# Optimization experiments

Hardware: AMD Instinct MI355X
Metric: run time of the kernel (lower is better)

The kernel has to match this reference:

```python
import jax, jax.numpy as jnp
import numpy as np

D_MODEL = 512
D_STATE = 128
D_CONV = 4
EXPAND = 2
NL = 10
HEADDIM = 64
D_INNER = EXPAND * D_MODEL            # 1024
NHEADS = D_INNER // HEADDIM           # 16
CONV_DIM = D_INNER + 2 * D_STATE      # 1280
D_PROJ = 2 * D_INNER + 2 * D_STATE + NHEADS  # 2320
BATCH = 8
IN_S, TOK_S = 3647, 64                # -> 57 tokens
IN_G, TOK_G = 18, 2                   # -> 9 tokens
NCLS = 55
CA_HEADS = 8
EPS = 1e-5


def setup_inputs() -> dict:
    key = jax.random.key(0)
    ks = iter(jax.random.split(key, 80))
    nrm = lambda shape, s=0.02: jax.random.normal(next(ks), shape, jnp.float32) * s
    inp = {
        "x_spectra": jax.random.normal(next(ks), (BATCH, IN_S), jnp.float32),
        "x_gaia": jax.random.normal(next(ks), (BATCH, IN_G), jnp.float32),
        "tok_w_s": nrm((TOK_S, D_MODEL), 0.05), "tok_b_s": jnp.zeros((D_MODEL,)),
        "tok_w_g": nrm((TOK_G, D_MODEL), 0.05), "tok_b_g": jnp.zeros((D_MODEL,)),
    }
    for p in ("ms", "mg"):  # spectra / gaia Mamba2 stacks, params stacked over layers
        inp[p + "_Win"] = nrm((NL, D_MODEL, D_PROJ))
        inp[p + "_conv_w"] = nrm((NL, CONV_DIM, D_CONV), 0.1)
        inp[p + "_conv_b"] = jnp.zeros((NL, CONV_DIM))
        inp[p + "_dt_bias"] = nrm((NL, NHEADS), 0.5)
        inp[p + "_A_log"] = jnp.log(jnp.tile(jnp.arange(1, NHEADS + 1, dtype=jnp.float32), (NL, 1)))
        inp[p + "_D"] = jnp.ones((NL, NHEADS))
        inp[p + "_norm_w"] = jnp.ones((NL, D_INNER))
        inp[p + "_Wout"] = nrm((NL, D_INNER, D_MODEL))
    for p in ("ca_s", "ca_g"):  # cross-attention blocks
        inp[p + "_ln_w"] = jnp.ones((D_MODEL,)); inp[p + "_ln_b"] = jnp.zeros((D_MODEL,))
        inp[p + "_in_w"] = nrm((3 * D_MODEL, D_MODEL)); inp[p + "_in_b"] = jnp.zeros((3 * D_MODEL,))
        inp[p + "_out_w"] = nrm((D_MODEL, D_MODEL)); inp[p + "_out_b"] = jnp.zeros((D_MODEL,))
    inp["cls_ln_w"] = jnp.ones((2 * D_MODEL,)); inp["cls_ln_b"] = jnp.zeros((2 * D_MODEL,))
    inp["cls_w"] = nrm((NCLS, 2 * D_MODEL)); inp["cls_b"] = jnp.zeros((NCLS,))
    return inp


def _ln(x, w, b):
    m = x.mean(-1, keepdims=True)
    v = jnp.var(x, -1, keepdims=True)
    return (x - m) * jax.lax.rsqrt(v + EPS) * w + b


def _tokenize(x, in_dim, tok_dim, w, b):
    bsz = x.shape[0]
    ntok = -(-in_dim // tok_dim)
    x = jnp.pad(x, ((0, 0), (0, ntok * tok_dim - in_dim)))
    return x.reshape(bsz, ntok, tok_dim) @ w + b  # [B, ntok, d_model]


def _mamba2_layer(x, Win, conv_w, conv_b, dt_bias, A_log, Dp, norm_w, Wout):
    bsz, L, _ = x.shape
    zxbcdt = x @ Win  # [B,L,D_PROJ]
    z, xBC, dt = jnp.split(zxbcdt, [D_INNER, D_INNER + CONV_DIM], axis=-1)
    # causal depthwise conv over time (kernel D_CONV), then SiLU
    xp = jnp.pad(xBC, ((0, 0), (D_CONV - 1, 0), (0, 0)))
    xBC = sum(conv_w[:, k] * xp[:, k:k + L, :] for k in range(D_CONV)) + conv_b
    xBC = jax.nn.silu(xBC)
    xh, Bm, Cm = jnp.split(xBC, [D_INNER, D_INNER + D_STATE], axis=-1)
    dt = jax.nn.softplus(dt + dt_bias)                 # [B,L,H]
    A = -jnp.exp(A_log)                                # [H]
    xh = xh.reshape(bsz, L, NHEADS, HEADDIM)
    dA = jnp.exp(dt * A)                               # [B,L,H] in (0,1)
    dBx = jnp.einsum('blh,bln,blhp->blhpn', dt, Bm, xh)
    # h_t = dA_t * h_{t-1} + dBx_t  via parallel associative scan over time
    def comb(e1, e2):
        a1, b1 = e1
        a2, b2 = e2
        return a1 * a2, a2[..., None, None] * b1 + b2
    _, h = jax.lax.associative_scan(comb, (dA, dBx), axis=1)  # h: [B,L,H,P,N]
    y = jnp.einsum('blhpn,bln->blhp', h, Cm) + Dp[None, None, :, None] * xh
    y = y.reshape(bsz, L, D_INNER)
    # gated RMSNorm (norm_before_gate=False): rmsnorm(y * silu(z)) * w
    y = y * jax.nn.silu(z)
    y = y * jax.lax.rsqrt(jnp.mean(y * y, -1, keepdims=True) + EPS) * norm_w
    return y @ Wout


def _mamba_stack(x, Win, cw, cb, dtb, Alog, Dp, nw, Wout):
    for i in range(NL):
        x = _mamba2_layer(x, Win[i], cw[i], cb[i], dtb[i], Alog[i], Dp[i], nw[i], Wout[i])
    return x


def _mha(q, kv, in_w, in_b, out_w, out_b):
    E = D_MODEL
    hd = E // CA_HEADS
    wq, wk, wv = in_w[:E], in_w[E:2 * E], in_w[2 * E:]
    bq, bk, bv = in_b[:E], in_b[E:2 * E], in_b[2 * E:]
    qh = (q @ wq.T + bq).reshape(*q.shape[:2], CA_HEADS, hd)
    kh = (kv @ wk.T + bk).reshape(*kv.shape[:2], CA_HEADS, hd)
    vh = (kv @ wv.T + bv).reshape(*kv.shape[:2], CA_HEADS, hd)
    scores = jnp.einsum('bqhd,bkhd->bhqk', qh, kh) / np.sqrt(hd).astype(np.float32)
    attn = jax.nn.softmax(scores, axis=-1)
    out = jnp.einsum('bhqk,bkhd->bqhd', attn, vh).reshape(*q.shape[:2], E)
    return out @ out_w.T + out_b


def reference(x_spectra, x_gaia, tok_w_s, tok_b_s, tok_w_g, tok_b_g,
              ms_Win, ms_conv_w, ms_conv_b, ms_dt_bias, ms_A_log, ms_D, ms_norm_w, ms_Wout,
              mg_Win, mg_conv_w, mg_conv_b, mg_dt_bias, mg_A_log, mg_D, mg_norm_w, mg_Wout,
              ca_s_ln_w, ca_s_ln_b, ca_s_in_w, ca_s_in_b, ca_s_out_w, ca_s_out_b,
              ca_g_ln_w, ca_g_ln_b, ca_g_in_w, ca_g_in_b, ca_g_out_w, ca_g_out_b,
              cls_ln_w, cls_ln_b, cls_w, cls_b):
    xs = _tokenize(x_spectra, IN_S, TOK_S, tok_w_s, tok_b_s)   # [B,57,512]
    xg = _tokenize(x_gaia, IN_G, TOK_G, tok_w_g, tok_b_g)      # [B,9,512]
    xs = _mamba_stack(xs, ms_Win, ms_conv_w, ms_conv_b, ms_dt_bias, ms_A_log, ms_D, ms_norm_w, ms_Wout)
    xg = _mamba_stack(xg, mg_Win, mg_conv_w, mg_conv_b, mg_dt_bias, mg_A_log, mg_D, mg_norm_w, mg_Wout)
    # cross attention (note: gaia attends to the UPDATED spectra, as in the torch code)
    xs = xs + _mha(_ln(xs, ca_s_ln_w, ca_s_ln_b), xg, ca_s_in_w, ca_s_in_b, ca_s_out_w, ca_s_out_b)
    xg = xg + _mha(_ln(xg, ca_g_ln_w, ca_g_ln_b), xs, ca_g_in_w, ca_g_in_b, ca_g_out_w, ca_g_out_b)
    fused = jnp.concatenate([xs.mean(1), xg.mean(1)], axis=-1)  # [B,1024]
    return _ln(fused, cls_ln_w, cls_ln_b) @ cls_w.T + cls_b      # [B,55]
```

## Files before the change

kernel.cpp:

```cpp
#include <hip/hip_runtime.h>
#include <cmath>

constexpr int BB    = 8;
constexpr int LS    = 57;
constexpr int LG    = 9;
constexpr int RS    = BB*LS;
constexpr int RG    = BB*LG;
constexpr int DM    = 512;
constexpr int DPROJ = 2320;
constexpr int DIN   = 1024;
constexpr int NH    = 16;
constexpr int HD    = 64;
constexpr int NLAY  = 10;

constexpr int SP_IN  = 2;
constexpr int SP_OUT = 8;
constexpr int SP_ATT = 4;

__device__ __forceinline__ float siluf(float x){ return x / (1.f + expf(-x)); }

typedef short  short8  __attribute__((ext_vector_type(8)));
typedef short  short4_ __attribute__((ext_vector_type(4)));
typedef float  f32x4   __attribute__((ext_vector_type(4)));

__device__ __forceinline__ unsigned short f2bh(float f){
    unsigned int u = __float_as_uint(f);
    u = u + 0x7FFFu + ((u >> 16) & 1u);
    return (unsigned short)(u >> 16);
}
__device__ __forceinline__ float bh2f(unsigned short h){
    return __uint_as_float(((unsigned int)h) << 16);
}

__global__ __launch_bounds__(512) void tokenize2(
    const float* __restrict__ xS, const float* __restrict__ wS, const float* __restrict__ bS,
    float* __restrict__ oS, unsigned short* __restrict__ oSh, unsigned short* __restrict__ oSl,
    const float* __restrict__ xG, const float* __restrict__ wG, const float* __restrict__ bG,
    float* __restrict__ oG, unsigned short* __restrict__ oGh, unsigned short* __restrict__ oGl)
{
    const int st = blockIdx.z;
    const int tkt = blockIdx.x, b = blockIdx.y, d = threadIdx.x;
    const int ntok = st ? LG : LS;
    if (tkt >= ntok) return;
    const float* x = st ? xG : xS;
    const float* w = st ? wG : wS;
    const float* bias = st ? bG : bS;
    float* out = st ? oG : oS;
    unsigned short* oh = st ? oGh : oSh;
    unsigned short* ol = st ? oGl : oSl;
    const int in_dim = st ? 18 : 3647, tok_dim = st ? 2 : 64;

    __shared__ float xv[64];
    if (d < tok_dim) {
        int idx = tkt*tok_dim + d;
        xv[d] = (idx < in_dim) ? x[(size_t)b*in_dim + idx] : 0.f;
    }
    __syncthreads();
    float acc = bias[d];
    for (int k=0;k<tok_dim;k++) acc += xv[k]*w[(size_t)k*DM + d];
    const size_t o = (size_t)(b*ntok + tkt)*DM + d;
    out[o] = acc;
    const unsigned short h = f2bh(acc);
    oh[o] = h;
    ol[o] = f2bh(acc - bh2f(h));
}

struct CvtE { const float* src; unsigned short* h; unsigned short* l; int nblk; };

__global__ __launch_bounds__(256) void convert_weights(
    const float* __restrict__ winS, const float* __restrict__ winG,
    const float* __restrict__ woutS, const float* __restrict__ woutG,
    unsigned short* __restrict__ winh, unsigned short* __restrict__ winl,
    unsigned short* __restrict__ wouth, unsigned short* __restrict__ woutl,
    CvtE e0, CvtE e1, CvtE e2, CvtE e3)
{
    __shared__ float tile[64][65];
    const int tid = threadIdx.x;
    const int bid = blockIdx.x;

    const float* src; unsigned short *dh, *dl; int K, N, nt, kt;
    if (bid < 5920){
        const int plane = bid / 296, rem = bid % 296;
        const int s = plane & 1, layer = plane >> 1;
        src = (s ? winG : winS) + (size_t)layer*DM*DPROJ;
        dh = winh + (size_t)plane*DPROJ*DM;
        dl = winl + (size_t)plane*DPROJ*DM;
        K = DM; N = DPROJ;
        nt = (rem % 37)*64; kt = (rem / 37)*64;
    } else if (bid < 8480){
        const int i = bid - 5920;
        const int plane = i / 128, rem = i % 128;
        const int s = plane & 1, layer = plane >> 1;
        src = (s ? woutG : woutS) + (size_t)layer*DIN*DM;
        dh = wouth + (size_t)plane*DM*DIN;
        dl = woutl + (size_t)plane*DM*DIN;
        K = DIN; N = DM;
        nt = (rem % 8)*64; kt = (rem / 8)*64;
    } else {
        int e = bid - 8480;
        CvtE j;
        if (e < e0.nblk){ j = e0; }
        else if (e < e0.nblk + e1.nblk){ j = e1; e -= e0.nblk; }
        else if (e < e0.nblk + e1.nblk + e2.nblk){ j = e2; e -= e0.nblk + e1.nblk; }
        else { j = e3; e -= e0.nblk + e1.nblk + e2.nblk; }
        const int i4 = (e*256 + tid)*4;
        const float4 v = *(const float4*)(j.src + i4);
        const float f[4] = {v.x,v.y,v.z,v.w};
        short4_ h4, l4;
        #pragma unroll
        for (int q=0;q<4;q++){
            const unsigned short h = f2bh(f[q]);
            h4[q] = (short)h;
            l4[q] = (short)f2bh(f[q] - bh2f(h));
        }
        *(short4_*)(j.h + i4) = h4;
        *(short4_*)(j.l + i4) = l4;
        return;
    }

    #pragma unroll
    for (int i=0;i<4;i++){
        const int kk = (tid>>4) + i*16;
        const int c4 = (tid&15)*4;
        const int n = nt + c4;
        float4 v = {0.f,0.f,0.f,0.f};
        if (n + 3 < N) v = *(const float4*)(src + (size_t)(kt+kk)*N + n);
        else {
            if (n   < N) v.x = src[(size_t)(kt+kk)*N + n];
            if (n+1 < N) v.y = src[(size_t)(kt+kk)*N + n+1];
            if (n+2 < N) v.z = src[(size_t)(kt+kk)*N + n+2];
            if (n+3 < N) v.w = src[(size_t)(kt+kk)*N + n+3];
        }
        tile[kk][c4]=v.x; tile[kk][c4+1]=v.y; tile[kk][c4+2]=v.z; tile[kk][c4+3]=v.w;
    }
    __syncthreads();
    #pragma unroll
    for (int i=0;i<2;i++){
        const int c = tid + i*256;
        const int n = c >> 3, k8 = (c & 7)*8;
        if (nt + n < N){
            short8 vh_, vl_;
            #pragma unroll
            for (int q=0;q<8;q++){
                const float f = tile[k8+q][n];
                const unsigned short h = f2bh(f);
                vh_[q] = (short)h;
                vl_[q] = (short)f2bh(f - bh2f(h));
            }
            *(short8*)(dh + (size_t)(nt+n)*K + kt + k8) = vh_;
            *(short8*)(dl + (size_t)(nt+n)*K + kt + k8) = vl_;
        }
    }
}

struct GemmJob {
    const unsigned short* Ah; const unsigned short* Al;
    const unsigned short* Wh; const unsigned short* Wl;
    float* part; int M;
};

template<int NSPLIT>
__global__ __launch_bounds__(256) void gemm_mfma(GemmJob j0, GemmJob j1, GemmJob j2, int N, int K)
{
    const int z = blockIdx.z;
    const int job = z / NSPLIT, split = z % NSPLIT;
    GemmJob jb = (job==0) ? j0 : (job==1 ? j1 : j2);
    const int bm = blockIdx.y*64, bn = blockIdx.x*64;
    const int M = jb.M;
    if (bm >= M) return;

    constexpr int SR = 40;
    __shared__ unsigned short AhS[2][64*SR], AlS[2][64*SR];
    __shared__ unsigned short BhS[2][64*SR], BlS[2][64*SR];

    const int tid = threadIdx.x;
    const int r0 = tid >> 2, k0off = (tid & 3)*8;
    const bool aok = (bm + r0 < M);
    const bool wok = (bn + r0 < N);
    const unsigned short* Aph = jb.Ah + (size_t)(bm+r0)*K;
    const unsigned short* Apl = jb.Al + (size_t)(bm+r0)*K;
    const unsigned short* Wph = jb.Wh + (size_t)(bn+r0)*K;
    const unsigned short* Wpl = jb.Wl + (size_t)(bn+r0)*K;

    const short8 z8 = {0,0,0,0,0,0,0,0};
    short8 ra_h = z8, ra_l = z8, rw_h = z8, rw_l = z8;

    auto loadT = [&](int k0){
        if (aok){
            ra_h = *(const short8*)(Aph + k0 + k0off);
            ra_l = *(const short8*)(Apl + k0 + k0off);
        } else { ra_h = z8; ra_l = z8; }
        if (wok){
            rw_h = *(const short8*)(Wph + k0 + k0off);
            rw_l = *(const short8*)(Wpl + k0 + k0off);
        } else { rw_h = z8; rw_l = z8; }
    };
    auto storeT = [&](int buf){
        *(short8*)&AhS[buf][r0*SR + k0off] = ra_h;
        *(short8*)&AlS[buf][r0*SR + k0off] = ra_l;
        *(short8*)&BhS[buf][r0*SR + k0off] = rw_h;
        *(short8*)&BlS[buf][r0*SR + k0off] = rw_l;
    };

    const int Kper = K / NSPLIT;
    const int koff = split * Kper;
    const int nk = Kper / 32;

    const int l = tid & 63, w = tid >> 6;
    const int fr = l & 15, kg = (l >> 4)*8;

    f32x4 acc0 = {0.f,0.f,0.f,0.f};
    f32x4 acc1 = {0.f,0.f,0.f,0.f};
    f32x4 acc2 = {0.f,0.f,0.f,0.f};
    f32x4 acc3 = {0.f,0.f,0.f,0.f};

    loadT(koff);
    storeT(0);
    __syncthreads();
    for (int t=0; t<nk; ++t){
        const int cur = t & 1;
        if (t+1 < nk) loadT(koff + (t+1)*32);

        const short8 ah = *(const short8*)&AhS[cur][(w*16+fr)*SR + kg];
        const short8 al = *(const short8*)&AlS[cur][(w*16+fr)*SR + kg];
        {
            const short8 bh = *(const short8*)&BhS[cur][(fr)*SR + kg];
            const short8 bl = *(const short8*)&BlS[cur][(fr)*SR + kg];
            acc0 = __builtin_amdgcn_mfma_f32_16x16x32_bf16(ah, bh, acc0, 0,0,0);
            acc0 = __builtin_amdgcn_mfma_f32_16x16x32_bf16(ah, bl, acc0, 0,0,0);
            acc0 = __builtin_amdgcn_mfma_f32_16x16x32_bf16(al, bh, acc0, 0,0,0);
        }
        {
            const short8 bh = *(const short8*)&BhS[cur][(16+fr)*SR + kg];
            const short8 bl = *(const short8*)&BlS[cur][(16+fr)*SR + kg];
            acc1 = __builtin_amdgcn_mfma_f32_16x16x32_bf16(ah, bh, acc1, 0,0,0);
            acc1 = __builtin_amdgcn_mfma_f32_16x16x32_bf16(ah, bl, acc1, 0,0,0);
            acc1 = __builtin_amdgcn_mfma_f32_16x16x32_bf16(al, bh, acc1, 0,0,0);
        }
        {
            const short8 bh = *(const short8*)&BhS[cur][(32+fr)*SR + kg];
            const short8 bl = *(const short8*)&BlS[cur][(32+fr)*SR + kg];
            acc2 = __builtin_amdgcn_mfma_f32_16x16x32_bf16(ah, bh, acc2, 0,0,0);
            acc2 = __builtin_amdgcn_mfma_f32_16x16x32_bf16(ah, bl, acc2, 0,0,0);
            acc2 = __builtin_amdgcn_mfma_f32_16x16x32_bf16(al, bh, acc2, 0,0,0);
        }
        {
            const short8 bh = *(const short8*)&BhS[cur][(48+fr)*SR + kg];
            const short8 bl = *(const short8*)&BlS[cur][(48+fr)*SR + kg];
            acc3 = __builtin_amdgcn_mfma_f32_16x16x32_bf16(ah, bh, acc3, 0,0,0);
            acc3 = __builtin_amdgcn_mfma_f32_16x16x32_bf16(ah, bl, acc3, 0,0,0);
            acc3 = __builtin_amdgcn_mfma_f32_16x16x32_bf16(al, bh, acc3, 0,0,0);
        }
        if (t+1 < nk) storeT(cur^1);
        __syncthreads();
    }

    float* __restrict__ P = jb.part + (size_t)split*M*N;
    const int rbase = bm + w*16 + (l>>4)*4;
    #pragma unroll
    for (int nt=0; nt<4; ++nt){
        const f32x4 a = (nt==0)?acc0 : (nt==1)?acc1 : (nt==2)?acc2 : acc3;
        const int n = bn + nt*16 + fr;
        if (n < N){
            #pragma unroll
            for (int j=0;j<4;j++){
                const int m = rbase + j;
                if (m < M) P[(size_t)m*N + n] = a[j];
            }
        }
    }
}

struct RJob { const float* part; const float* bias; const float* res; float* C;
              unsigned short* ph; unsigned short* pl; int M; };

template<int NS>
__global__ __launch_bounds__(256) void reduce_k(RJob j0, RJob j1, int N)
{
    RJob j = blockIdx.y ? j1 : j0;
    const size_t total = (size_t)j.M*N;
    const size_t i4 = ((size_t)blockIdx.x*256 + threadIdx.x)*4;
    if (i4 >= total) return;
    float4 s = *(const float4*)(j.part + i4);
    #pragma unroll
    for (int t=1;t<NS;t++){
        const float4 v = *(const float4*)(j.part + (size_t)t*total + i4);
        s.x+=v.x; s.y+=v.y; s.z+=v.z; s.w+=v.w;
    }
    const int n = (int)(i4 % (size_t)N);
    if (j.bias){ s.x+=j.bias[n]; s.y+=j.bias[n+1]; s.z+=j.bias[n+2]; s.w+=j.bias[n+3]; }
    if (j.res){ const float4 r = *(const float4*)(j.res + i4); s.x+=r.x; s.y+=r.y; s.z+=r.z; s.w+=r.w; }
    if (j.C) *(float4*)(j.C + i4) = s;
    if (j.ph){
        const float f[4] = {s.x, s.y, s.z, s.w};
        short4_ h4, l4;
        #pragma unroll
        for (int q=0;q<4;q++){
            const unsigned short h = f2bh(f[q]);
            h4[q] = (short)h;
            l4[q] = (short)f2bh(f[q] - bh2f(h));
        }
        *(short4_*)(j.ph + i4) = h4;
        *(short4_*)(j.pl + i4) = l4;
    }
}

struct PrepJob {
    const float* part;
    float* zsilu; float* xh; float* Bc; float* Cc; float* dtw;
    const float* cw; const float* cb; const float* dtb;
    int R, L;
};

__device__ __forceinline__ float4 psum2(const float* p, size_t pstr){
    float4 a = *(const float4*)p;
    const float4 b = *(const float4*)(p + pstr);
    a.x += b.x; a.y += b.y; a.z += b.z; a.w += b.w;
    return a;
}

__global__ __launch_bounds__(256) void mamba_prep(PrepJob js, PrepJob jg)
{
    PrepJob j = blockIdx.y ? jg : js;
    const int R = j.R, L = j.L;
    constexpr int QPR = 580;
    const int q = blockIdx.x*256 + threadIdx.x;
    if (q >= R*QPR) return;
    const int r = q / QPR, qi = q % QPR;
    const int l = r % L;
    const size_t pstr = (size_t)R*DPROJ;
    const float* base = j.part + (size_t)r*DPROJ;

    if (qi < 256) {
        const int c = qi*4;
        float4 s = psum2(base + c, pstr);
        s.x = siluf(s.x); s.y = siluf(s.y); s.z = siluf(s.z); s.w = siluf(s.w);
        *(float4*)(j.zsilu + (size_t)r*1024 + c) = s;
    } else if (qi < 576) {
        const int cc = (qi-256)*4;
        float tk[4][4];
        #pragma unroll
        for (int k=0;k<4;k++){
            const int lr = l - 3 + k;
            if (lr >= 0){
                float4 v = psum2(j.part + (size_t)(r-3+k)*DPROJ + 1024 + cc, pstr);
                tk[k][0]=v.x; tk[k][1]=v.y; tk[k][2]=v.z; tk[k][3]=v.w;
            } else {
                tk[k][0]=0.f; tk[k][1]=0.f; tk[k][2]=0.f; tk[k][3]=0.f;
            }
        }
        const float4 cb4 = *(const float4*)(j.cb + cc);
        const float cba[4] = {cb4.x, cb4.y, cb4.z, cb4.w};
        float out[4];
        #pragma unroll
        for (int jj=0;jj<4;jj++){
            const float4 wv = *(const float4*)(j.cw + (size_t)(cc+jj)*4);
            float v = cba[jj] + wv.x*tk[0][jj] + wv.y*tk[1][jj]
                              + wv.z*tk[2][jj] + wv.w*tk[3][jj];
            out[jj] = siluf(v);
        }
        float4 o4; o4.x=out[0]; o4.y=out[1]; o4.z=out[2]; o4.w=out[3];
        if (cc < 1024)       *(float4*)(j.xh + (size_t)r*1024 + cc)        = o4;
        else if (cc < 1152)  *(float4*)(j.Bc + (size_t)r*128 + (cc-1024))  = o4;
        else                 *(float4*)(j.Cc + (size_t)r*128 + (cc-1152))  = o4;
    } else {
        const int hd = (qi-576)*4;
        float4 s = psum2(base + 2304 + hd, pstr);
        const float4 b4 = *(const float4*)(j.dtb + hd);
        float raw[4] = {s.x+b4.x, s.y+b4.y, s.z+b4.z, s.w+b4.w};
        float4 o4;
        float* op = &o4.x;
        #pragma unroll
        for (int jj=0;jj<4;jj++)
            op[jj] = (raw[jj] > 20.f) ? raw[jj] : log1pf(expf(raw[jj]));
        *(float4*)(j.dtw + (size_t)r*16 + hd) = o4;
    }
}

__global__ __launch_bounds__(256) void mamba_cbt(
    const float* __restrict__ Bc_s, const float* __restrict__ Cc_s, float* __restrict__ cbt_s,
    const float* __restrict__ Bc_g, const float* __restrict__ Cc_g, float* __restrict__ cbt_g)
{
    const int b = blockIdx.x, st = blockIdx.y;
    const float* Bc = st ? Bc_g : Bc_s;
    const float* Cc = st ? Cc_g : Cc_s;
    float* cbt = st ? cbt_g : cbt_s;
    const int L = st ? LG : LS;
    constexpr int SB = 132;
    __shared__ float Bm[64*SB], Cm[64*SB];
    const int t = threadIdx.x;
    for (int idx = t; idx < L*32; idx += 256){
        const int l = idx >> 5, c4 = (idx & 31)*4;
        *(float4*)&Bm[l*SB + c4] = *(const float4*)(Bc + (size_t)(b*L+l)*128 + c4);
        *(float4*)&Cm[l*SB + c4] = *(const float4*)(Cc + (size_t)(b*L+l)*128 + c4);
    }
    __syncthreads();
    const int ti = t >> 4, tj = t & 15;
    float acc[4][4] = {};
    for (int k0=0;k0<128;k0+=4){
        float4 cr[4], br[4];
        #pragma unroll
        for (int a=0;a<4;a++) cr[a] = *(const float4*)&Cm[(ti+16*a)*SB + k0];
        #pragma unroll
        for (int qq=0;qq<4;qq++) br[qq] = *(const float4*)&Bm[(tj+16*qq)*SB + k0];
        #pragma unroll
        for (int a=0;a<4;a++)
            #pragma unroll
            for (int qq=0;qq<4;qq++)
                acc[a][qq] += cr[a].x*br[qq].x + cr[a].y*br[qq].y
                            + cr[a].z*br[qq].z + cr[a].w*br[qq].w;
    }
    #pragma unroll
    for (int a=0;a<4;a++){
        const int i = ti + 16*a;
        if (i < L){
            #pragma unroll
            for (int qq=0;qq<4;qq++){
                const int jj = tj + 16*qq;
                if (jj < L) cbt[(size_t)b*3840 + i*60 + jj] = acc[a][qq];
// ... 40 lines not shown
        *(float4*)&Xm[l*SX + c4] = *(const float4*)(xh + (size_t)(b*L+l)*1024 + h*64 + c4);
    }
    __syncthreads();

    for (int idx = t; idx < L*15; idx += 256){
        const int i = idx/15, j4 = (idx%15)*4;
        const float4 v = *(const float4*)(cbt + (size_t)b*3840 + i*60 + j4);
        const float va[4] = {v.x, v.y, v.z, v.w};
        float g[4];
        const float si = sps[i];
        #pragma unroll
        for (int jj=0;jj<4;jj++){
            const int jc = j4 + jj;
            float gg = 0.f;
            if (jc <= i && jc < L)
                gg = expf(Ah*(si - sps[jc])) * dts[jc] * va[jj];
            g[jj] = gg;
        }
        float4 g4; g4.x=g[0]; g4.y=g[1]; g4.z=g[2]; g4.w=g[3];
        *(float4*)&Gm[i*SG + j4] = g4;
    }
    __syncthreads();

    const int ti = t >> 4, tj = t & 15;
    int la[4];
    #pragma unroll
    for (int a=0;a<4;a++) la[a] = ti + 16*a;
    float accY[4][4] = {};
    for (int m=0; m<L; ++m){
        float xr[4], gr[4];
        #pragma unroll
        for (int qq=0;qq<4;qq++) xr[qq] = Xm[m*SX + tj + 16*qq];
        #pragma unroll
        for (int a=0;a<4;a++) gr[a] = (la[a] < L) ? Gm[la[a]*SG + m] : 0.f;
        #pragma unroll
        for (int a=0;a<4;a++)
            #pragma unroll
            for (int qq=0;qq<4;qq++) accY[a][qq] = fmaf(gr[a], xr[qq], accY[a][qq]);
    }
    #pragma unroll
    for (int a=0;a<4;a++){
        if (la[a] < L){
            float* yrow = y + (size_t)(b*L + la[a])*DIN + h*HD;
            #pragma unroll
            for (int qq=0;qq<4;qq++){
                const int col = tj + 16*qq;
                yrow[col] = accY[a][qq] + Dh * Xm[la[a]*SX + col];
            }
        }
    }
}

__global__ __launch_bounds__(256) void gated_rmsnorm(
    const float* __restrict__ y_s, const float* __restrict__ zs_s, const float* __restrict__ nw_s,
    unsigned short* __restrict__ oh_s, unsigned short* __restrict__ ol_s,
    const float* __restrict__ y_g, const float* __restrict__ zs_g, const float* __restrict__ nw_g,
    unsigned short* __restrict__ oh_g, unsigned short* __restrict__ ol_g)
{
    int r = blockIdx.x, t = threadIdx.x;
    int st = (r >= RS);
    int row = st ? r - RS : r;
    const float* y  = (st ? y_g  : y_s) + (size_t)row*DIN;
    const float* zs = (st ? zs_g : zs_s) + (size_t)row*DIN;
    const float* nw = st ? nw_g : nw_s;
    unsigned short* oh = (st ? oh_g : oh_s) + (size_t)row*DIN;
    unsigned short* ol = (st ? ol_g : ol_s) + (size_t)row*DIN;

    float g[4]; float s2 = 0.f;
    #pragma unroll
    for (int i=0;i<4;i++){
        int idx = t + i*256;
        float gv = y[idx] * zs[idx];
        g[i] = gv; s2 += gv*gv;
    }
    #pragma unroll
    for (int o2=32;o2;o2>>=1) s2 += __shfl_xor(s2, o2, 64);
    __shared__ float red[4];
    if ((t & 63) == 0) red[t>>6] = s2;
    __syncthreads();
    float S2 = red[0]+red[1]+red[2]+red[3];
    float scale = rsqrtf(S2*(1.f/DIN) + 1e-5f);
    #pragma unroll
    for (int i=0;i<4;i++){
        int idx = t + i*256;
        const float val = g[i]*scale*nw[idx];
        const unsigned short h = f2bh(val);
        oh[idx] = h;
        ol[idx] = f2bh(val - bh2f(h));
    }
}

__global__ __launch_bounds__(256) void ln_rows(
    const float* __restrict__ x, const float* __restrict__ w, const float* __restrict__ b,
    unsigned short* __restrict__ outh, unsigned short* __restrict__ outl, int D)
{
    int r = blockIdx.x, t = threadIdx.x;
    const float* xr = x + (size_t)r*D;
    float s = 0.f, s2 = 0.f;
    for (int i=t;i<D;i+=256){ float v = xr[i]; s += v; s2 += v*v; }
    #pragma unroll
    for (int o=32;o;o>>=1){ s += __shfl_xor(s,o,64); s2 += __shfl_xor(s2,o,64); }
    __shared__ float red[8];
    if ((t & 63) == 0){ red[t>>6] = s; red[4+(t>>6)] = s2; }
    __syncthreads();
    float S  = red[0]+red[1]+red[2]+red[3];
    float S2 = red[4]+red[5]+red[6]+red[7];
    float mean = S/D;
    float var  = S2/D - mean*mean;
    float inv  = rsqrtf(var + 1e-5f);
    for (int i=t;i<D;i+=256){
        const float val = (xr[i]-mean)*inv*w[i] + b[i];
        const unsigned short h = f2bh(val);
        outh[(size_t)r*D + i] = h;
        outl[(size_t)r*D + i] = f2bh(val - bh2f(h));
    }
}

template<int LQ, int LKV, int NS>
__global__ __launch_bounds__(256) void mha_attn2(
    const float* __restrict__ pq, const float* __restrict__ pk, const float* __restrict__ pv,
    const float* __restrict__ qb, const float* __restrict__ kb, const float* __restrict__ vb,
    int Mq, int Mkv,
    unsigned short* __restrict__ outh, unsigned short* __restrict__ outl)
{
    const int hh = blockIdx.x, b = blockIdx.y, t = threadIdx.x;
// ... 182 lines not shown
    (void)in_sizes; (void)n_in; (void)out_size; (void)ws_size;
    const float* x_spectra = (const float*)d_in[0];
    const float* x_gaia    = (const float*)d_in[1];
    const float* tok_w_s   = (const float*)d_in[2];
    const float* tok_b_s   = (const float*)d_in[3];
    const float* tok_w_g   = (const float*)d_in[4];
    const float* tok_b_g   = (const float*)d_in[5];
    const float* ms_Win    = (const float*)d_in[6];
    const float* ms_conv_w = (const float*)d_in[7];
    const float* ms_conv_b = (const float*)d_in[8];
    const float* ms_dtb    = (const float*)d_in[9];
    const float* ms_Alog   = (const float*)d_in[10];
    const float* ms_D      = (const float*)d_in[11];
    const float* ms_nw     = (const float*)d_in[12];
    const float* ms_Wout   = (const float*)d_in[13];
    const float* mg_Win    = (const float*)d_in[14];
    const float* mg_conv_w = (const float*)d_in[15];
    const float* mg_conv_b = (const float*)d_in[16];
    const float* mg_dtb    = (const float*)d_in[17];
    const float* mg_Alog   = (const float*)d_in[18];
    const float* mg_D      = (const float*)d_in[19];
    const float* mg_nw     = (const float*)d_in[20];
    const float* mg_Wout   = (const float*)d_in[21];
    const float* cas_ln_w  = (const float*)d_in[22];
    const float* cas_ln_b  = (const float*)d_in[23];
    const float* cas_in_w  = (const float*)d_in[24];
    const float* cas_in_b  = (const float*)d_in[25];
    const float* cas_out_w = (const float*)d_in[26];
    const float* cas_out_b = (const float*)d_in[27];
    const float* cag_ln_w  = (const float*)d_in[28];
    const float* cag_ln_b  = (const float*)d_in[29];
    const float* cag_in_w  = (const float*)d_in[30];
    const float* cag_in_b  = (const float*)d_in[31];
    const float* cag_out_w = (const float*)d_in[32];
    const float* cag_out_b = (const float*)d_in[33];
    const float* cls_ln_w  = (const float*)d_in[34];
    const float* cls_ln_b  = (const float*)d_in[35];
    const float* cls_w     = (const float*)d_in[36];
    const float* cls_b     = (const float*)d_in[37];

    float* p = (float*)d_ws;
    auto alloc = [&](size_t n){ float* r = p; p += n; return r; };
    float* xs       = alloc((size_t)RS*DM);
    float* xg       = alloc((size_t)RG*DM);
    float* y_s      = alloc((size_t)RS*DIN);
    float* y_g      = alloc((size_t)RG*DIN);
    float* part_inS  = alloc((size_t)SP_IN*RS*DPROJ);
    float* part_inG  = alloc((size_t)SP_IN*RG*DPROJ);
    float* part_outS = alloc((size_t)SP_OUT*RS*DM);
    float* part_outG = alloc((size_t)SP_OUT*RG*DM);
    float* part_q    = alloc((size_t)SP_ATT*RS*DM);
    float* part_k    = alloc((size_t)SP_ATT*RS*DM);
    float* part_v    = alloc((size_t)SP_ATT*RS*DM);
    float* zsilu_s = alloc((size_t)RS*1024);
    float* zsilu_g = alloc((size_t)RG*1024);
    float* xh_s    = alloc((size_t)RS*1024);
    float* xh_g    = alloc((size_t)RG*1024);
    float* Bc_s    = alloc((size_t)RS*128);
    float* Bc_g    = alloc((size_t)RG*128);
    float* Cc_s    = alloc((size_t)RS*128);
    float* Cc_g    = alloc((size_t)RG*128);
    float* dtw_s   = alloc((size_t)RS*16);
    float* dtw_g   = alloc((size_t)RG*16);
    float* cbt_s   = alloc((size_t)BB*3840);
    float* cbt_g   = alloc((size_t)BB*3840);

    unsigned short* up = (unsigned short*)p;
    auto ualloc = [&](size_t n){ unsigned short* r = up; up += n; return r; };
    unsigned short* xsh   = ualloc((size_t)RS*DM);
    unsigned short* xsl   = ualloc((size_t)RS*DM);
    unsigned short* xgh   = ualloc((size_t)RG*DM);
    unsigned short* xgl   = ualloc((size_t)RG*DM);
    unsigned short* ynh_s = ualloc((size_t)RS*DIN);
    unsigned short* ynl_s = ualloc((size_t)RS*DIN);
    unsigned short* ynh_g = ualloc((size_t)RG*DIN);
    unsigned short* ynl_g = ualloc((size_t)RG*DIN);
    unsigned short* lnh   = ualloc((size_t)RS*DM);
    unsigned short* lnl   = ualloc((size_t)RS*DM);
    unsigned short* aoh   = ualloc((size_t)RS*DM);
    unsigned short* aol   = ualloc((size_t)RS*DM);
    unsigned short* caih  = ualloc((size_t)1536*512);
    unsigned short* cail  = ualloc((size_t)1536*512);
    unsigned short* caoh  = ualloc((size_t)512*512);
    unsigned short* caol  = ualloc((size_t)512*512);
    unsigned short* cgih  = ualloc((size_t)1536*512);
    unsigned short* cgil  = ualloc((size_t)1536*512);
    unsigned short* cgoh  = ualloc((size_t)512*512);
    unsigned short* cgol  = ualloc((size_t)512*512);
    unsigned short* winh  = ualloc((size_t)20*DPROJ*DM);
    unsigned short* winl  = ualloc((size_t)20*DPROJ*DM);
    unsigned short* wouth = ualloc((size_t)20*DM*DIN);
    unsigned short* woutl = ualloc((size_t)20*DM*DIN);

    CvtE e0{cas_in_w,  caih, cail, 768};
    CvtE e1{cas_out_w, caoh, caol, 256};
    CvtE e2{cag_in_w,  cgih, cgil, 768};
    CvtE e3{cag_out_w, cgoh, cgol, 256};
    convert_weights<<<dim3(10528), 256, 0, stream>>>(
        ms_Win, mg_Win, ms_Wout, mg_Wout, winh, winl, wouth, woutl, e0, e1, e2, e3);

    tokenize2<<<dim3(LS, BB, 2), 512, 0, stream>>>(
        x_spectra, tok_w_s, tok_b_s, xs, xsh, xsl,
        x_gaia,    tok_w_g, tok_b_g, xg, xgh, xgl);

    const int rblkS = (RS*DM + 1023)/1024;
    const int prepBlk = (RS*580 + 255)/256;

    for (int i=0;i<NLAY;i++){
        const float* cw_s   = ms_conv_w + (size_t)i*1280*4;
        const float* cw_g   = mg_conv_w + (size_t)i*1280*4;
        const float* cbv_s  = ms_conv_b + (size_t)i*1280;
        const float* cbv_g  = mg_conv_b + (size_t)i*1280;
        const float* dtb_s  = ms_dtb  + (size_t)i*NH;
        const float* dtb_g  = mg_dtb  + (size_t)i*NH;
        const float* al_s   = ms_Alog + (size_t)i*NH;
        const float* al_g   = mg_Alog + (size_t)i*NH;
        const float* Dw_s   = ms_D    + (size_t)i*NH;
        const float* Dw_g   = mg_D    + (size_t)i*NH;
        const float* nw_s   = ms_nw   + (size_t)i*DIN;
        const float* nw_g   = mg_nw   + (size_t)i*DIN;

        const unsigned short* wih_s = winh + (size_t)(2*i+0)*DPROJ*DM;
        const unsigned short* wil_s = winl + (size_t)(2*i+0)*DPROJ*DM;
        const unsigned short* wih_g = winh + (size_t)(2*i+1)*DPROJ*DM;
        const unsigned short* wil_g = winl + (size_t)(2*i+1)*DPROJ*DM;
        const unsigned short* woh_s = wouth + (size_t)(2*i+0)*DM*DIN;
        const unsigned short* wol_s = woutl + (size_t)(2*i+0)*DM*DIN;
        const unsigned short* woh_g = wouth + (size_t)(2*i+1)*DM*DIN;
        const unsigned short* wol_g = woutl + (size_t)(2*i+1)*DM*DIN;

        GemmJob inS{xsh, xsl, wih_s, wil_s, part_inS, RS};
        GemmJob inG{xgh, xgl, wih_g, wil_g, part_inG, RG};
        gemm_mfma<SP_IN><<<dim3(37, 8, 2*SP_IN), 256, 0, stream>>>(inS, inG, inG, DPROJ, DM);

        PrepJob pjS{part_inS, zsilu_s, xh_s, Bc_s, Cc_s, dtw_s, cw_s, cbv_s, dtb_s, RS, LS};
        PrepJob pjG{part_inG, zsilu_g, xh_g, Bc_g, Cc_g, dtw_g, cw_g, cbv_g, dtb_g, RG, LG};
        mamba_prep<<<dim3(prepBlk, 2), 256, 0, stream>>>(pjS, pjG);

        mamba_cbt<<<dim3(BB, 2), 256, 0, stream>>>(Bc_s, Cc_s, cbt_s, Bc_g, Cc_g, cbt_g);

        mamba_y<<<dim3(NH, BB, 2), 256, 0, stream>>>(
            cbt_s, xh_s, dtw_s, al_s, Dw_s, y_s,
            cbt_g, xh_g, dtw_g, al_g, Dw_g, y_g);

        gated_rmsnorm<<<dim3(RS+RG), 256, 0, stream>>>(
            y_s, zsilu_s, nw_s, ynh_s, ynl_s,  y_g, zsilu_g, nw_g, ynh_g, ynl_g);

        GemmJob outS{ynh_s, ynl_s, woh_s, wol_s, part_outS, RS};
        GemmJob outG{ynh_g, ynl_g, woh_g, wol_g, part_outG, RG};
        gemm_mfma<SP_OUT><<<dim3(8, 8, 2*SP_OUT), 256, 0, stream>>>(outS, outG, outG, DM, DIN);

        RJob roS{part_outS, nullptr, nullptr, xs, xsh, xsl, RS};
        RJob roG{part_outG, nullptr, nullptr, xg, xgh, xgl, RG};
        reduce_k<SP_OUT><<<dim3(rblkS, 2), 256, 0, stream>>>(roS, roG, DM);
    }

    {
        ln_rows<<<dim3(RS), 256, 0, stream>>>(xs, cas_ln_w, cas_ln_b, lnh, lnl, DM);
        GemmJob jq{lnh, lnl, caih,            cail,            part_q, RS};
        GemmJob jk{xgh, xgl, caih +  512*512, cail +  512*512, part_k, RG};
        GemmJob jv{xgh, xgl, caih + 1024*512, cail + 1024*512, part_v, RG};
        gemm_mfma<SP_ATT><<<dim3(8, 8, 3*SP_ATT), 256, 0, stream>>>(jq, jk, jv, DM, DM);
        mha_attn2<LS,LG,SP_ATT><<<dim3(8,BB), 256, 0, stream>>>(
            part_q, part_k, part_v, cas_in_b, cas_in_b+512, cas_in_b+1024, RS, RG, aoh, aol);
        GemmJob jo{aoh, aol, caoh, caol, part_outS, RS};
        gemm_mfma<SP_ATT><<<dim3(8, 8, SP_ATT), 256, 0, stream>>>(jo, jo, jo, DM, DM);
        RJob ro{part_outS, cas_out_b, xs, xs, xsh, xsl, RS};
        reduce_k<SP_ATT><<<dim3(rblkS, 1), 256, 0, stream>>>(ro, ro, DM);
    }

    {
        ln_rows<<<dim3(RG), 256, 0, stream>>>(xg, cag_ln_w, cag_ln_b, lnh, lnl, DM);
        GemmJob jq{lnh, lnl, cgih,            cgil,            part_q, RG};
        GemmJob jk{xsh, xsl, cgih +  512*512, cgil +  512*512, part_k, RS};
        GemmJob jv{xsh, xsl, cgih + 1024*512, cgil + 1024*512, part_v, RS};
        gemm_mfma<SP_ATT><<<dim3(8, 8, 3*SP_ATT), 256, 0, stream>>>(jq, jk, jv, DM, DM);
        mha_attn2<LG,LS,SP_ATT><<<dim3(8,BB), 256, 0, stream>>>(
            part_q, part_k, part_v, cag_in_b, cag_in_b+512, cag_in_b+1024, RG, RS, aoh, aol);
        GemmJob jo{aoh, aol, cgoh, cgol, part_outS, RG};
        gemm_mfma<SP_ATT><<<dim3(8, 2, SP_ATT), 256, 0, stream>>>(jo, jo, jo, DM, DM);
        RJob ro{part_outS, cag_out_b, xg, xg, nullptr, nullptr, RG};
        reduce_k<SP_ATT><<<dim3((RG*DM+1023)/1024, 1), 256, 0, stream>>>(ro, ro, DM);
    }

    head_fused<<<dim3(BB), 512, 0, stream>>>(xs, xg, cls_ln_w, cls_ln_b, cls_w, cls_b, (float*)d_out);
}
```

Before: 749.7 us.

## Pre-tile bf16 weight planes for contiguous GEMM loads and fuse z-silu into rmsnorm

```diff
diff --git a/kernel.cpp b/kernel.cpp
--- a/kernel.cpp
+++ b/kernel.cpp
@@ -17,6 +17,13 @@
 constexpr int SP_OUT = 8;
 constexpr int SP_ATT = 4;
 
+constexpr int NT_IN  = 37;
+constexpr int NT_OUT = 8;
+constexpr int NT_ATT = 8;
+constexpr size_t WIN_PLANE  = (size_t)16*NT_IN*2048;
+constexpr size_t WOUT_PLANE = (size_t)32*NT_OUT*2048;
+constexpr size_t ATT_PLANE  = (size_t)16*NT_ATT*2048;
+
 __device__ __forceinline__ float siluf(float x){ return x / (1.f + expf(-x)); }
 
 typedef short  short8  __attribute__((ext_vector_type(8)));
@@ -65,91 +72,97 @@
     ol[o] = f2bh(acc - bh2f(h));
 }
 
-struct CvtE { const float* src; unsigned short* h; unsigned short* l; int nblk; };
-
 __global__ __launch_bounds__(256) void convert_weights(
     const float* __restrict__ winS, const float* __restrict__ winG,
     const float* __restrict__ woutS, const float* __restrict__ woutG,
+    const float* __restrict__ cai, const float* __restrict__ cao,
+    const float* __restrict__ cgi, const float* __restrict__ cgo,
     unsigned short* __restrict__ winh, unsigned short* __restrict__ winl,
     unsigned short* __restrict__ wouth, unsigned short* __restrict__ woutl,
-    CvtE e0, CvtE e1, CvtE e2, CvtE e3)
-{
-    __shared__ float tile[64][65];
+    unsigned short* __restrict__ atth, unsigned short* __restrict__ attl)
+{
     const int tid = threadIdx.x;
     const int bid = blockIdx.x;
 
-    const float* src; unsigned short *dh, *dl; int K, N, nt, kt;
+    if (bid >= 8480){
+        int e = bid - 8480;
+        const int job = e >> 7, rem = e & 127;
+        const int kt2 = rem >> 3, nt2 = rem & 7;
+        const float* src =
+            (job==3) ? cao : (job==7) ? cgo :
+            (job< 3) ? cai + (size_t)job*512*512 : cgi + (size_t)(job-4)*512*512;
+        const size_t tile = (size_t)job*ATT_PLANE + ((size_t)kt2*NT_ATT + nt2)*2048;
+        const int n = tid >> 2, k8 = (tid & 3)*8;
+        const float* sp = src + (size_t)(nt2*64 + n)*512 + kt2*32 + k8;
+        const float4 v0 = *(const float4*)sp;
+        const float4 v1 = *(const float4*)(sp+4);
+        const float f[8] = {v0.x,v0.y,v0.z,v0.w,v1.x,v1.y,v1.z,v1.w};
+        short8 h8, l8;
+        #pragma unroll
+        for (int q=0;q<8;q++){
+            const unsigned short h = f2bh(f[q]);
+            h8[q] = (short)h;
+            l8[q] = (short)f2bh(f[q] - bh2f(h));
+        }
+        *(short8*)(atth + tile + tid*8) = h8;
+        *(short8*)(attl + tile + tid*8) = l8;
+        return;
+    }
+
+    const float* src; unsigned short *dh, *dl; int K, N, NT, nt, ktp;
     if (bid < 5920){
         const int plane = bid / 296, rem = bid % 296;
         const int s = plane & 1, layer = plane >> 1;
         src = (s ? winG : winS) + (size_t)layer*DM*DPROJ;
-        dh = winh + (size_t)plane*DPROJ*DM;
-        dl = winl + (size_t)plane*DPROJ*DM;
-        K = DM; N = DPROJ;
-        nt = (rem % 37)*64; kt = (rem / 37)*64;
-    } else if (bid < 8480){
+        dh = winh + (size_t)plane*WIN_PLANE;
+        dl = winl + (size_t)plane*WIN_PLANE;
+        K = DM; N = DPROJ; NT = NT_IN;
+        nt = rem % 37; ktp = rem / 37;
+    } else {
         const int i = bid - 5920;
         const int plane = i / 128, rem = i % 128;
         const int s = plane & 1, layer = plane >> 1;
         src = (s ? woutG : woutS) + (size_t)layer*DIN*DM;
-        dh = wouth + (size_t)plane*DM*DIN;
-        dl = woutl + (size_t)plane*DM*DIN;
-        K = DIN; N = DM;
-        nt = (rem % 8)*64; kt = (rem / 8)*64;
-    } else {
-        int e = bid - 8480;
-        CvtE j;
-        if (e < e0.nblk){ j = e0; }
-        else if (e < e0.nblk + e1.nblk){ j = e1; e -= e0.nblk; }
-        else if (e < e0.nblk + e1.nblk + e2.nblk){ j = e2; e -= e0.nblk + e1.nblk; }
-        else { j = e3; e -= e0.nblk + e1.nblk + e2.nblk; }
-        const int i4 = (e*256 + tid)*4;
-        const float4 v = *(const float4*)(j.src + i4);
-        const float f[4] = {v.x,v.y,v.z,v.w};
-        short4_ h4, l4;
-        #pragma unroll
-        for (int q=0;q<4;q++){
-            const unsigned short h = f2bh(f[q]);
-            h4[q] = (short)h;
-            l4[q] = (short)f2bh(f[q] - bh2f(h));
-        }
-        *(short4_*)(j.h + i4) = h4;
-        *(short4_*)(j.l + i4) = l4;
-        return;
-    }
-
+        dh = wouth + (size_t)plane*WOUT_PLANE;
+        dl = woutl + (size_t)plane*WOUT_PLANE;
+        K = DIN; N = DM; NT = NT_OUT;
+        nt = rem % 8; ktp = rem / 8;
+    }
+
+    __shared__ float tile[64][66];
     #pragma unroll
     for (int i=0;i<4;i++){
         const int kk = (tid>>4) + i*16;
         const int c4 = (tid&15)*4;
-        const int n = nt + c4;
+        const int n = nt*64 + c4;
         float4 v = {0.f,0.f,0.f,0.f};
-        if (n + 3 < N) v = *(const float4*)(src + (size_t)(kt+kk)*N + n);
+        const float* sp = src + (size_t)(ktp*64+kk)*N + n;
+        if (n + 3 < N) v = *(const float4*)sp;
         else {
-            if (n   < N) v.x = src[(size_t)(kt+kk)*N + n];
-            if (n+1 < N) v.y = src[(size_t)(kt+kk)*N + n+1];
-            if (n+2 < N) v.z = src[(size_t)(kt+kk)*N + n+2];
-            if (n+3 < N) v.w = src[(size_t)(kt+kk)*N + n+3];
+            if (n   < N) v.x = sp[0];
+            if (n+1 < N) v.y = sp[1];
+            if (n+2 < N) v.z = sp[2];
+            if (n+3 < N) v.w = sp[3];
         }
         tile[kk][c4]=v.x; tile[kk][c4+1]=v.y; tile[kk][c4+2]=v.z; tile[kk][c4+3]=v.w;
     }
     __syncthreads();
+
+    const int n_l = tid >> 2, k8 = (tid & 3)*8;
     #pragma unroll
     for (int i=0;i<2;i++){
-        const int c = tid + i*256;
-        const int n = c >> 3, k8 = (c & 7)*8;
-        if (nt + n < N){
-            short8 vh_, vl_;
-            #pragma unroll
-            for (int q=0;q<8;q++){
-                const float f = tile[k8+q][n];
-                const unsigned short h = f2bh(f);
-                vh_[q] = (short)h;
-                vl_[q] = (short)f2bh(f - bh2f(h));
-            }
-            *(short8*)(dh + (size_t)(nt+n)*K + kt + k8) = vh_;
-            *(short8*)(dl + (size_t)(nt+n)*K + kt + k8) = vl_;
-        }
+        const int kt2 = ktp*2 + i;
+        short8 h8, l8;
+        #pragma unroll
+        for (int q=0;q<8;q++){
+            const float f = tile[i*32 + k8 + q][n_l];
+            const unsigned short h = f2bh(f);
+            h8[q] = (short)h;
+            l8[q] = (short)f2bh(f - bh2f(h));
+        }
+        const size_t off = ((size_t)kt2*NT + nt)*2048 + tid*8;
+        *(short8*)(dh + off) = h8;
+        *(short8*)(dl + off) = l8;
     }
 }
 
@@ -160,12 +173,13 @@
 };
 
 template<int NSPLIT>
-__global__ __launch_bounds__(256) void gemm_mfma(GemmJob j0, GemmJob j1, GemmJob j2, int N, int K)
+__global__ __launch_bounds__(256) void gemm_mfma(GemmJob j0, GemmJob j1, GemmJob j2,
+                                                 int N, int K, int NT)
 {
     const int z = blockIdx.z;
     const int job = z / NSPLIT, split = z % NSPLIT;
     GemmJob jb = (job==0) ? j0 : (job==1 ? j1 : j2);
-    const int bm = blockIdx.y*64, bn = blockIdx.x*64;
+    const int bm = blockIdx.y*64, bn64 = blockIdx.x;
     const int M = jb.M;
     if (bm >= M) return;
 
@@ -176,24 +190,26 @@
     const int tid = threadIdx.x;
     const int r0 = tid >> 2, k0off = (tid & 3)*8;
     const bool aok = (bm + r0 < M);
-    const bool wok = (bn + r0 < N);
     const unsigned short* Aph = jb.Ah + (size_t)(bm+r0)*K;
     const unsigned short* Apl = jb.Al + (size_t)(bm+r0)*K;
-    const unsigned short* Wph = jb.Wh + (size_t)(bn+r0)*K;
-    const unsigned short* Wpl = jb.Wl + (size_t)(bn+r0)*K;
+
+    const int Kper = K / NSPLIT;
+    const int koff = split * Kper;
+    const int nk = Kper / 32;
+
+    const size_t wbase = ((size_t)(koff >> 5)*NT + bn64)*2048 + (size_t)tid*8;
+    const size_t wstep = (size_t)NT*2048;
 
     const short8 z8 = {0,0,0,0,0,0,0,0};
     short8 ra_h = z8, ra_l = z8, rw_h = z8, rw_l = z8;
 
-    auto loadT = [&](int k0){
+    auto loadT = [&](int k0, int tstep){
         if (aok){
             ra_h = *(const short8*)(Aph + k0 + k0off);
             ra_l = *(const short8*)(Apl + k0 + k0off);
         } else { ra_h = z8; ra_l = z8; }
-        if (wok){
-            rw_h = *(const short8*)(Wph + k0 + k0off);
-            rw_l = *(const short8*)(Wpl + k0 + k0off);
-        } else { rw_h = z8; rw_l = z8; }
+        rw_h = *(const short8*)(jb.Wh + wbase + (size_t)tstep*wstep);
+        rw_l = *(const short8*)(jb.Wl + wbase + (size_t)tstep*wstep);
     };
     auto storeT = [&](int buf){
         *(short8*)&AhS[buf][r0*SR + k0off] = ra_h;
@@ -202,10 +218,6 @@
         *(short8*)&BlS[buf][r0*SR + k0off] = rw_l;
     };
 
-    const int Kper = K / NSPLIT;
-    const int koff = split * Kper;
-    const int nk = Kper / 32;
-
     const int l = tid & 63, w = tid >> 6;
     const int fr = l & 15, kg = (l >> 4)*8;
 
@@ -214,12 +226,12 @@
     f32x4 acc2 = {0.f,0.f,0.f,0.f};
     f32x4 acc3 = {0.f,0.f,0.f,0.f};
 
-    loadT(koff);
+    loadT(koff, 0);
     storeT(0);
     __syncthreads();
     for (int t=0; t<nk; ++t){
         const int cur = t & 1;
-        if (t+1 < nk) loadT(koff + (t+1)*32);
+        if (t+1 < nk) loadT(koff + (t+1)*32, t+1);
 
         const short8 ah = *(const short8*)&AhS[cur][(w*16+fr)*SR + kg];
         const short8 al = *(const short8*)&AlS[cur][(w*16+fr)*SR + kg];
@@ -257,6 +269,7 @@
 
     float* __restrict__ P = jb.part + (size_t)split*M*N;
     const int rbase = bm + w*16 + (l>>4)*4;
+    const int bn = bn64*64;
     #pragma unroll
     for (int nt=0; nt<4; ++nt){
         const f32x4 a = (nt==0)?acc0 : (nt==1)?acc1 : (nt==2)?acc2 : acc3;
@@ -307,7 +320,7 @@
 
 struct PrepJob {
     const float* part;
-    float* zsilu; float* xh; float* Bc; float* Cc; float* dtw;
+    float* xh; float* Bc; float* Cc; float* dtw;
     const float* cw; const float* cb; const float* dtb;
     int R, L;
 };
@@ -323,7 +336,7 @@
 {
     PrepJob j = blockIdx.y ? jg : js;
     const int R = j.R, L = j.L;
-    constexpr int QPR = 580;
+    constexpr int QPR = 324;
     const int q = blockIdx.x*256 + threadIdx.x;
     if (q >= R*QPR) return;
     const int r = q / QPR, qi = q % QPR;
@@ -331,13 +344,8 @@
     const size_t pstr = (size_t)R*DPROJ;
     const float* base = j.part + (size_t)r*DPROJ;
 
-    if (qi < 256) {
-        const int c = qi*4;
-        float4 s = psum2(base + c, pstr);
-        s.x = siluf(s.x); s.y = siluf(s.y); s.z = siluf(s.z); s.w = siluf(s.w);
-        *(float4*)(j.zsilu + (size_t)r*1024 + c) = s;
-    } else if (qi < 576) {
-        const int cc = (qi-256)*4;
+    if (qi < 320) {
+        const int cc = qi*4;
         float tk[4][4];
         #pragma unroll
         for (int k=0;k<4;k++){
@@ -364,7 +372,7 @@
         else if (cc < 1152)  *(float4*)(j.Bc + (size_t)r*128 + (cc-1024))  = o4;
         else                 *(float4*)(j.Cc + (size_t)r*128 + (cc-1152))  = o4;
     } else {
-        const int hd = (qi-576)*4;
+        const int hd = (qi-320)*4;
         float4 s = psum2(base + 2304 + hd, pstr);
         const float4 b4 = *(const float4*)(j.dtb + hd);
         float raw[4] = {s.x+b4.x, s.y+b4.y, s.z+b4.z, s.w+b4.w};
@@ -511,16 +519,17 @@
 }
 
 __global__ __launch_bounds__(256) void gated_rmsnorm(
-    const float* __restrict__ y_s, const float* __restrict__ zs_s, const float* __restrict__ nw_s,
+    const float* __restrict__ y_s, const float* __restrict__ part_s, const float* __restrict__ nw_s,
     unsigned short* __restrict__ oh_s, unsigned short* __restrict__ ol_s,
-    const float* __restrict__ y_g, const float* __restrict__ zs_g, const float* __restrict__ nw_g,
+    const float* __restrict__ y_g, const float* __restrict__ part_g, const float* __restrict__ nw_g,
     unsigned short* __restrict__ oh_g, unsigned short* __restrict__ ol_g)
 {
     int r = blockIdx.x, t = threadIdx.x;
     int st = (r >= RS);
     int row = st ? r - RS : r;
     const float* y  = (st ? y_g  : y_s) + (size_t)row*DIN;
-    const float* zs = (st ? zs_g : zs_s) + (size_t)row*DIN;
+    const float* zp = (st ? part_g : part_s) + (size_t)row*DPROJ;
+    const size_t pstr = (size_t)(st ? RG : RS)*DPROJ;
     const float* nw = st ? nw_g : nw_s;
     unsigned short* oh = (st ? oh_g : oh_s) + (size_t)row*DIN;
     unsigned short* ol = (st ? ol_g : ol_s) + (size_t)row*DIN;
@@ -529,7 +538,8 @@
     #pragma unroll
     for (int i=0;i<4;i++){
         int idx = t + i*256;
-        float gv = y[idx] * zs[idx];
+        const float zv = zp[idx] + zp[pstr + idx];
+        float gv = y[idx] * siluf(zv);
         g[i] = gv; s2 += gv*gv;
     }
     #pragma unroll
@@ -818,8 +828,6 @@
     float* part_q    = alloc((size_t)SP_ATT*RS*DM);
     float* part_k    = alloc((size_t)SP_ATT*RS*DM);
     float* part_v    = alloc((size_t)SP_ATT*RS*DM);
-    float* zsilu_s = alloc((size_t)RS*1024);
-    float* zsilu_g = alloc((size_t)RG*1024);
     float* xh_s    = alloc((size_t)RS*1024);
     float* xh_g    = alloc((size_t)RG*1024);
     float* Bc_s    = alloc((size_t)RS*128);
@@ -845,32 +853,33 @@
     unsigned short* lnl   = ualloc((size_t)RS*DM);
     unsigned short* aoh   = ualloc((size_t)RS*DM);
     unsigned short* aol   = ualloc((size_t)RS*DM);
-    unsigned short* caih  = ualloc((size_t)1536*512);
-    unsigned short* cail  = ualloc((size_t)1536*512);
-    unsigned short* caoh  = ualloc((size_t)512*512);
-    unsigned short* caol  = ualloc((size_t)512*512);
-    unsigned short* cgih  = ualloc((size_t)1536*512);
-    unsigned short* cgil  = ualloc((size_t)1536*512);
-    unsigned short* cgoh  = ualloc((size_t)512*512);
-    unsigned short* cgol  = ualloc((size_t)512*512);
-    unsigned short* winh  = ualloc((size_t)20*DPROJ*DM);
-    unsigned short* winl  = ualloc((size_t)20*DPROJ*DM);
-    unsigned short* wouth = ualloc((size_t)20*DM*DIN);
-    unsigned short* woutl = ualloc((size_t)20*DM*DIN);
-
-    CvtE e0{cas_in_w,  caih, cail, 768};
-    CvtE e1{cas_out_w, caoh, caol, 256};
-    CvtE e2{cag_in_w,  cgih, cgil, 768};
-    CvtE e3{cag_out_w, cgoh, cgol, 256};
-    convert_weights<<<dim3(10528), 256, 0, stream>>>(
-        ms_Win, mg_Win, ms_Wout, mg_Wout, winh, winl, wouth, woutl, e0, e1, e2, e3);
+    unsigned short* atth  = ualloc((size_t)8*ATT_PLANE);
+    unsigned short* attl  = ualloc((size_t)8*ATT_PLANE);
+    unsigned short* winh  = ualloc((size_t)20*WIN_PLANE);
+    unsigned short* winl  = ualloc((size_t)20*WIN_PLANE);
+    unsigned short* wouth = ualloc((size_t)20*WOUT_PLANE);
+    unsigned short* woutl = ualloc((size_t)20*WOUT_PLANE);
+
+    unsigned short* casq_h = atth + 0*ATT_PLANE; unsigned short* casq_l = attl + 0*ATT_PLANE;
+    unsigned short* cask_h = atth + 1*ATT_PLANE; unsigned short* cask_l = attl + 1*ATT_PLANE;
+    unsigned short* casv_h = atth + 2*ATT_PLANE; unsigned short* casv_l = attl + 2*ATT_PLANE;
+    unsigned short* caso_h = atth + 3*ATT_PLANE; unsigned short* caso_l = attl + 3*ATT_PLANE;
+    unsigned short* cagq_h = atth + 4*ATT_PLANE; unsigned short* cagq_l = attl + 4*ATT_PLANE;
+    unsigned short* cagk_h = atth + 5*ATT_PLANE; unsigned short* cagk_l = attl + 5*ATT_PLANE;
+    unsigned short* cagv_h = atth + 6*ATT_PLANE; unsigned short* cagv_l = attl + 6*ATT_PLANE;
+    unsigned short* cago_h = atth + 7*ATT_PLANE; unsigned short* cago_l = attl + 7*ATT_PLANE;
+
+    convert_weights<<<dim3(9504), 256, 0, stream>>>(
+        ms_Win, mg_Win, ms_Wout, mg_Wout,
+        cas_in_w, cas_out_w, cag_in_w, cag_out_w,
+        winh, winl, wouth, woutl, atth, attl);
 
     tokenize2<<<dim3(LS, BB, 2), 512, 0, stream>>>(
         x_spectra, tok_w_s, tok_b_s, xs, xsh, xsl,
         x_gaia,    tok_w_g, tok_b_g, xg, xgh, xgl);
 
     const int rblkS = (RS*DM + 1023)/1024;
-    const int prepBlk = (RS*580 + 255)/256;
+    const int prepBlk = (RS*324 + 255)/256;
 
     for (int i=0;i<NLAY;i++){
         const float* cw_s   = ms_conv_w + (size_t)i*1280*4;
@@ -886,21 +895,22 @@
         const float* nw_s   = ms_nw   + (size_t)i*DIN;
         const float* nw_g   = mg_nw   + (size_t)i*DIN;
 
-        const unsigned short* wih_s = winh + (size_t)(2*i+0)*DPROJ*DM;
-        const unsigned short* wil_s = winl + (size_t)(2*i+0)*DPROJ*DM;
-        const unsigned short* wih_g = winh + (size_t)(2*i+1)*DPROJ*DM;
-        const unsigned short* wil_g = winl + (size_t)(2*i+1)*DPROJ*DM;
-        const unsigned short* woh_s = wouth + (size_t)(2*i+0)*DM*DIN;
-        const unsigned short* wol_s = woutl + (size_t)(2*i+0)*DM*DIN;
-        const unsigned short* woh_g = wouth + (size_t)(2*i+1)*DM*DIN;
-        const unsigned short* wol_g = woutl + (size_t)(2*i+1)*DM*DIN;
+        const unsigned short* wih_s = winh + (size_t)(2*i+0)*WIN_PLANE;
+        const unsigned short* wil_s = winl + (size_t)(2*i+0)*WIN_PLANE;
+        const unsigned short* wih_g = winh + (size_t)(2*i+1)*WIN_PLANE;
+        const unsigned short* wil_g = winl + (size_t)(2*i+1)*WIN_PLANE;
+        const unsigned short* woh_s = wouth + (size_t)(2*i+0)*WOUT_PLANE;
+        const unsigned short* wol_s = woutl + (size_t)(2*i+0)*WOUT_PLANE;
+        const unsigned short* woh_g = wouth + (size_t)(2*i+1)*WOUT_PLANE;
+        const unsigned short* wol_g = woutl + (size_t)(2*i+1)*WOUT_PLANE;
 
         GemmJob inS{xsh, xsl, wih_s, wil_s, part_inS, RS};
         GemmJob inG{xgh, xgl, wih_g, wil_g, part_inG, RG};
-        gemm_mfma<SP_IN><<<dim3(37, 8, 2*SP_IN), 256, 0, stream>>>(inS, inG, inG, DPROJ, DM);
-
-        PrepJob pjS{part_inS, zsilu_s, xh_s, Bc_s, Cc_s, dtw_s, cw_s, cbv_s, dtb_s, RS, LS};
-        PrepJob pjG{part_inG, zsilu_g, xh_g, Bc_g, Cc_g, dtw_g, cw_g, cbv_g, dtb_g, RG, LG};
+        gemm_mfma<SP_IN><<<dim3(NT_IN, 8, 2*SP_IN), 256, 0, stream>>>(
+            inS, inG, inG, DPROJ, DM, NT_IN);
+
+        PrepJob pjS{part_inS, xh_s, Bc_s, Cc_s, dtw_s, cw_s, cbv_s, dtb_s, RS, LS};
+        PrepJob pjG{part_inG, xh_g, Bc_g, Cc_g, dtw_g, cw_g, cbv_g, dtb_g, RG, LG};
         mamba_prep<<<dim3(prepBlk, 2), 256, 0, stream>>>(pjS, pjG);
 
         mamba_cbt<<<dim3(BB, 2), 256, 0, stream>>>(Bc_s, Cc_s, cbt_s, Bc_g, Cc_g, cbt_g);
@@ -910,11 +920,12 @@
             cbt_g, xh_g, dtw_g, al_g, Dw_g, y_g);
 
         gated_rmsnorm<<<dim3(RS+RG), 256, 0, stream>>>(
-            y_s, zsilu_s, nw_s, ynh_s, ynl_s,  y_g, zsilu_g, nw_g, ynh_g, ynl_g);
+            y_s, part_inS, nw_s, ynh_s, ynl_s,  y_g, part_inG, nw_g, ynh_g, ynl_g);
 
         GemmJob outS{ynh_s, ynl_s, woh_s, wol_s, part_outS, RS};
         GemmJob outG{ynh_g, ynl_g, woh_g, wol_g, part_outG, RG};
-        gemm_mfma<SP_OUT><<<dim3(8, 8, 2*SP_OUT), 256, 0, stream>>>(outS, outG, outG, DM, DIN);
+        gemm_mfma<SP_OUT><<<dim3(NT_OUT, 8, 2*SP_OUT), 256, 0, stream>>>(
+            outS, outG, outG, DM, DIN, NT_OUT);
 
         RJob roS{part_outS, nullptr, nullptr, xs, xsh, xsl, RS};
         RJob roG{part_outG, nullptr, nullptr, xg, xgh, xgl, RG};
@@ -923,28 +934,28 @@
 
     {
         ln_rows<<<dim3(RS), 256, 0, stream>>>(xs, cas_ln_w, cas_ln_b, lnh, lnl, DM);
-        GemmJob jq{lnh, lnl, caih,            cail,            part_q, RS};
-        GemmJob jk{xgh, xgl, caih +  512*512, cail +  512*512, part_k, RG};
-        GemmJob jv{xgh, xgl, caih + 1024*512, cail + 1024*512, part_v, RG};
-        gemm_mfma<SP_ATT><<<dim3(8, 8, 3*SP_ATT), 256, 0, stream>>>(jq, jk, jv, DM, DM);
+        GemmJob jq{lnh, lnl, casq_h, casq_l, part_q, RS};
+        GemmJob jk{xgh, xgl, cask_h, cask_l, part_k, RG};
+        GemmJob jv{xgh, xgl, casv_h, casv_l, part_v, RG};
+        gemm_mfma<SP_ATT><<<dim3(NT_ATT, 8, 3*SP_ATT), 256, 0, stream>>>(jq, jk, jv, DM, DM, NT_ATT);
         mha_attn2<LS,LG,SP_ATT><<<dim3(8,BB), 256, 0, stream>>>(
             part_q, part_k, part_v, cas_in_b, cas_in_b+512, cas_in_b+1024, RS, RG, aoh, aol);
-        GemmJob jo{aoh, aol, caoh, caol, part_outS, RS};
-        gemm_mfma<SP_ATT><<<dim3(8, 8, SP_ATT), 256, 0, stream>>>(jo, jo, jo, DM, DM);
+        GemmJob jo{aoh, aol, caso_h, caso_l, part_outS, RS};
+        gemm_mfma<SP_ATT><<<dim3(NT_ATT, 8, SP_ATT), 256, 0, stream>>>(jo, jo, jo, DM, DM, NT_ATT);
         RJob ro{part_outS, cas_out_b, xs, xs, xsh, xsl, RS};
         reduce_k<SP_ATT><<<dim3(rblkS, 1), 256, 0, stream>>>(ro, ro, DM);
     }
 
     {
         ln_rows<<<dim3(RG), 256, 0, stream>>>(xg, cag_ln_w, cag_ln_b, lnh, lnl, DM);
-        GemmJob jq{lnh, lnl, cgih,            cgil,            part_q, RG};
-        GemmJob jk{xsh, xsl, cgih +  512*512, cgil +  512*512, part_k, RS};
-        GemmJob jv{xsh, xsl, cgih + 1024*512, cgil + 1024*512, part_v, RS};
-        gemm_mfma<SP_ATT><<<dim3(8, 8, 3*SP_ATT), 256, 0, stream>>>(jq, jk, jv, DM, DM);
+        GemmJob jq{lnh, lnl, cagq_h, cagq_l, part_q, RG};
+        GemmJob jk{xsh, xsl, cagk_h, cagk_l, part_k, RS};
+        GemmJob jv{xsh, xsl, cagv_h, cagv_l, part_v, RS};
+        gemm_mfma<SP_ATT><<<dim3(NT_ATT, 8, 3*SP_ATT), 256, 0, stream>>>(jq, jk, jv, DM, DM, NT_ATT);
         mha_attn2<LG,LS,SP_ATT><<<dim3(8,BB), 256, 0, stream>>>(
             part_q, part_k, part_v, cag_in_b, cag_in_b+512, cag_in_b+1024, RG, RS, aoh, aol);
-        GemmJob jo{aoh, aol, cgoh, cgol, part_outS, RG};
-        gemm_mfma<SP_ATT><<<dim3(8, 2, SP_ATT), 256, 0, stream>>>(jo, jo, jo, DM, DM);
+        GemmJob jo{aoh, aol, cago_h, cago_l, part_outS, RG};
+        gemm_mfma<SP_ATT><<<dim3(NT_ATT, 2, SP_ATT), 256, 0, stream>>>(jo, jo, jo, DM, DM, NT_ATT);
         RJob ro{part_outS, cag_out_b, xg, xg, nullptr, nullptr, RG};
         reduce_k<SP_ATT><<<dim3((RG*DM+1023)/1024, 1), 256, 0, stream>>>(ro, ro, DM);
     }
```

Measured after the change: 733.0 us. -2.2%, faster.
